# Performance work log

Measured on AMD Instinct MI355X. Metric: run time of the kernel, lower is better.

## Reference

```python
import jax, jax.numpy as jnp
import numpy as np
from jax import lax

EPS = 1e-4  # BatchNorm eps from the module
K = 3       # kernel_size
PAD = 1     # padding


def setup_inputs() -> dict:
    key = jax.random.key(0)
    k1, k2, k3 = jax.random.split(key, 3)
    N, Cin, H, Wd = 32, 256, 56, 56
    Cout = 256
    x = jax.random.normal(k1, (N, Cin, H, Wd), dtype=jnp.float32)
    gamma = jnp.ones((Cin,), dtype=jnp.float32)
    beta_bn = jnp.zeros((Cin,), dtype=jnp.float32)
    W = jax.random.normal(k2, (Cout, Cin, K, K), dtype=jnp.float32) * 0.05
    b = jax.random.normal(k3, (Cout,), dtype=jnp.float32) * 0.01
    return {"x": x, "gamma": gamma, "beta_bn": beta_bn, "W": W, "b": b}


def _conv(x, w, padding):
    return lax.conv_general_dilated(
        x, w, window_strides=(1, 1),
        padding=[(padding, padding), (padding, padding)],
        dimension_numbers=("NCHW", "OIHW", "NCHW"))


def reference(x, gamma, beta_bn, W, b):
    # BatchNorm2d in training mode: batch statistics over (N, H, W), biased var
    mu = jnp.mean(x, axis=(0, 2, 3), keepdims=True)
    var = jnp.var(x, axis=(0, 2, 3), keepdims=True)
    xn = (x - mu) * lax.rsqrt(var + EPS)
    xn = xn * gamma[None, :, None, None] + beta_bn[None, :, None, None]

    # BinActiv: per-pixel channel-mean of |x|, then sign-binarize
    m = jnp.mean(jnp.abs(xn), axis=1, keepdims=True)  # [N,1,H,W]
    xb = jnp.sign(xn)

    # Binarize weights; alpha = L1 norm per output filter / n
    n = W.shape[1] * W.shape[2] * W.shape[3]
    alpha = jnp.sum(jnp.abs(W), axis=(1, 2, 3)) / n  # [Cout]
    Wb = jnp.sign(W)

    y = _conv(xb, Wb, PAD) + b[None, :, None, None]

    # beta map: box filter (stride 1) over channel-mean magnitudes
    box = jnp.full((1, 1, K, K), 1.0 / (K * K), dtype=x.dtype)
    beta_map = _conv(m, box, PAD)  # [N,1,Ho,Wo]

    out = jax.nn.relu(y * beta_map * alpha[None, :, None, None])
    return out
```

## Files before the change

### kernel.cpp

```cpp
#include <hip/hip_runtime.h>
#include <cstdint>
#include <cstddef>

#define N_    32
#define C_    256
#define H_    56
#define W_    56
#define HW_   (H_ * W_)
#define NHW_  (N_ * HW_)
#define COUT_ 256
#define EPS_  1e-4f

__global__ void k_bn_partial(const float* __restrict__ x,
                             float* __restrict__ ps, float* __restrict__ pq) {
    const int c = blockIdx.x >> 3;
    const int s = blockIdx.x & 7;
    const int t = threadIdx.x;
    float sm = 0.f, sq = 0.f;
    for (int n = s * 4; n < s * 4 + 4; ++n) {
        const float4* p = (const float4*)(x + (size_t)(n * C_ + c) * HW_);
        for (int i = t; i < HW_ / 4; i += 256) {
            float4 v = p[i];
            sm += v.x + v.y + v.z + v.w;
            sq += v.x * v.x + v.y * v.y + v.z * v.z + v.w * v.w;
        }
    }
    __shared__ float ls[256], lq[256];
    ls[t] = sm; lq[t] = sq;
    __syncthreads();
    for (int off = 128; off >= 1; off >>= 1) {
        if (t < off) { ls[t] += ls[t + off]; lq[t] += lq[t + off]; }
        __syncthreads();
    }
    if (t == 0) { ps[s * C_ + c] = ls[0]; pq[s * C_ + c] = lq[0]; }
}

__global__ void k_bn_final(const float* __restrict__ ps, const float* __restrict__ pq,
                           const float* __restrict__ gamma, const float* __restrict__ beta,
                           float* __restrict__ a, float* __restrict__ bb) {
    const int c = threadIdx.x;
    float sm = 0.f, sq = 0.f;
    for (int s = 0; s < 8; ++s) { sm += ps[s * C_ + c]; sq += pq[s * C_ + c]; }
    float mu   = sm * (1.f / NHW_);
    float var  = sq * (1.f / NHW_) - mu * mu;
    float rstd = rsqrtf(var + EPS_);
    float g    = gamma[c] * rstd;
    a[c]  = g;
    bb[c] = beta[c] - mu * g;
}

__global__ void k_wpack(const float* __restrict__ Wt, float* __restrict__ alpha,
                        uint64_t* __restrict__ wbits, int* __restrict__ wpopc) {
    const int co = blockIdx.x;
    const int ci = threadIdx.x;
    const int lane = ci & 63, wave = ci >> 6;
    const float* p = Wt + (size_t)(co * C_ + ci) * 9;
    float wv[9];
    float asum = 0.f;
#pragma unroll
    for (int t = 0; t < 9; ++t) { wv[t] = p[t]; asum += fabsf(wv[t]); }
    __shared__ int Pl[9];
    if (ci < 9) Pl[ci] = 0;
    __syncthreads();
#pragma unroll
    for (int t = 0; t < 9; ++t) {
        uint64_t mask = __ballot(wv[t] > 0.f);
        if (lane == 0) {
            wbits[(co * 9 + t) * 4 + wave] = mask;
            atomicAdd(&Pl[t], (int)__popcll(mask));
        }
    }
    __shared__ float red[256];
    red[ci] = asum;
    __syncthreads();
    for (int off = 128; off >= 1; off >>= 1) {
        if (ci < off) red[ci] += red[ci + off];
        __syncthreads();
    }
    if (ci == 0) alpha[co] = red[0] * (1.f / 2304.f);
    if (ci < 9) wpopc[co * 12 + ci] = Pl[ci];
}

__global__ void k_mpack(const float* __restrict__ x, const float* __restrict__ a,
                        const float* __restrict__ bb, uint64_t* __restrict__ xbits,
                        float* __restrict__ m) {
    const int p = blockIdx.x * 256 + threadIdx.x;
    const int n = p / HW_;
    const int hw = p - n * HW_;
    const float* xp = x + (size_t)n * C_ * HW_ + hw;
    float macc = 0.f;
    uint64_t bits[4];
#pragma unroll
    for (int wd = 0; wd < 4; ++wd) {
        uint64_t bw = 0;
#pragma unroll
        for (int j = 0; j < 64; ++j) {
            const int c = wd * 64 + j;
            float xn = fmaf(xp[(size_t)c * HW_], a[c], bb[c]);
            macc += fabsf(xn);
            bw |= (xn > 0.f) ? (1ull << j) : 0ull;
        }
        bits[wd] = bw;
    }
    ulonglong2* xb = (ulonglong2*)(xbits + (size_t)p * 4);
    xb[0] = make_ulonglong2(bits[0], bits[1]);
    xb[1] = make_ulonglong2(bits[2], bits[3]);
    m[p] = macc * (1.f / C_);
}

__global__ void k_box(const float* __restrict__ m, float* __restrict__ beta_map) {
    const int idx = blockIdx.x * 256 + threadIdx.x;
    if (idx >= NHW_) return;
    const int w = idx % W_;
    const int h = (idx / W_) % H_;
    const int n = idx / HW_;
    const float* mp = m + (size_t)n * HW_;
    float s = 0.f;
#pragma unroll
    for (int dh = 0; dh < 3; ++dh) {
        int ih = h + dh - 1;
        if (ih < 0 || ih >= H_) continue;
#pragma unroll
        for (int dw = 0; dw < 3; ++dw) {
            int iw = w + dw - 1;
            if (iw < 0 || iw >= W_) continue;
            s += mp[ih * W_ + iw];
        }
    }
    beta_map[idx] = s * (1.f / 9.f);
}

__global__ void __launch_bounds__(256)
k_conv(const uint64_t* __restrict__ xbits, const uint64_t* __restrict__ wbits,
       const int* __restrict__ wpopc,
       const float* __restrict__ beta_map, const float* __restrict__ alpha,
       const float* __restrict__ bias, float* __restrict__ out) {
    const int nh = blockIdx.x;
    const int n = nh / H_, h = nh % H_;
    const int lane = (int)(threadIdx.x & 63);
    const int wv = __builtin_amdgcn_readfirstlane((int)(threadIdx.x >> 6));
    const int w = lane;
    const bool r0 = (h > 0), r2 = (h < H_ - 1);

    bool cok0 = (w >= 1) && (w < W_);
    bool cok1 = (w < W_);
    bool cok2 = (w < W_ - 1);
    const int nvalid = (1 + (int)r0 + (int)r2) * ((int)cok0 + (int)cok1 + (int)cok2);

    uint64_t xw[9][4];
    const uint64_t* xim = xbits + (size_t)n * HW_ * 4;
#pragma unroll
    for (int dh = 0; dh < 3; ++dh) {
        const bool rok = (dh == 0) ? r0 : (dh == 2) ? r2 : true;
        int ih = h + dh - 1;
        ih = ih < 0 ? 0 : (ih > H_ - 1 ? H_ - 1 : ih);
#pragma unroll
        for (int dw = 0; dw < 3; ++dw) {
            const bool cok = (dw == 0) ? cok0 : (dw == 2) ? cok2 : cok1;
            int iw = w + dw - 1;
            iw = iw < 0 ? 0 : (iw > W_ - 1 ? W_ - 1 : iw);
            const uint64_t* xp = xim + ((size_t)ih * W_ + iw) * 4;
            const bool ok = rok && cok;
#pragma unroll
            for (int wd = 0; wd < 4; ++wd)
                xw[dh * 3 + dw][wd] = ok ? xp[wd] : 0ull;
        }
    }

    const float bm = (w < W_) ? beta_map[(size_t)n * HW_ + (size_t)h * W_ + w] : 0.f;
    float* obase = out + (size_t)n * COUT_ * HW_ + (size_t)h * W_;

    for (int coi = 0; coi < 64; ++coi) {
        const int co = wv * 64 + coi;
        const uint64_t* wq = wbits + (size_t)co * 36;
        const int* pq = wpopc + co * 12;

        int acc0 = 0, acc1 = 0, acc2 = 0, acc3 = 0;
#pragma unroll
        for (int t = 0; t < 9; ++t) {
            acc0 += __popcll(xw[t][0] ^ wq[t * 4 + 0]);
            acc1 += __popcll(xw[t][1] ^ wq[t * 4 + 1]);
            acc2 += __popcll(xw[t][2] ^ wq[t * 4 + 2]);
            acc3 += __popcll(xw[t][3] ^ wq[t * 4 + 3]);
        }
        const int acc = (acc0 + acc1) + (acc2 + acc3);

        int P[9], Ptot = 0;
#pragma unroll
        for (int t = 0; t < 9; ++t) { P[t] = pq[t]; Ptot += P[t]; }
        const int cs0 = (r0 ? P[0] : 0) + P[3] + (r2 ? P[6] : 0);
        const int cs1 = (r0 ? P[1] : 0) + P[4] + (r2 ? P[7] : 0);
        const int cs2 = (r0 ? P[2] : 0) + P[5] + (r2 ? P[8] : 0);
        const int sumv = (cok0 ? cs0 : 0) + (cok1 ? cs1 : 0) + (cok2 ? cs2 : 0);
        const int corr = Ptot - sumv;

        const int dot = 256 * nvalid - 2 * acc + 2 * corr;
        float o = ((float)dot + bias[co]) * bm * alpha[co];
        o = fmaxf(o, 0.f);
        if (w < W_) obase[(size_t)co * HW_ + w] = o;
    }
}

extern "C" void kernel_launch(void* const* d_in, const int* in_sizes, int n_in,
                              void* d_out, int out_size, void* d_ws, size_t ws_size,
                              hipStream_t stream) {
    (void)in_sizes; (void)n_in; (void)out_size; (void)ws_size;
    const float* x     = (const float*)d_in[0];
    const float* gamma = (const float*)d_in[1];
    const float* betab = (const float*)d_in[2];
    const float* Wt    = (const float*)d_in[3];
    const float* b     = (const float*)d_in[4];
    float* out = (float*)d_out;

    uint8_t* base = (uint8_t*)d_ws;
    float*    ps       = (float*)(base + 0);
    float*    pq       = (float*)(base + 8192);
    float*    a        = (float*)(base + 16384);
    float*    bb       = (float*)(base + 17408);
    float*    alpha    = (float*)(base + 18432);
    int*      wpopc    = (int*)(base + 19456);
    uint64_t* wbits    = (uint64_t*)(base + 31744);
    uint64_t* xbits    = (uint64_t*)(base + 105472);
    float*    m        = (float*)(base + 3316736);
    float*    beta_map = (float*)(base + 3718144);

    k_bn_partial<<<2048, 256, 0, stream>>>(x, ps, pq);
    k_bn_final<<<1, 256, 0, stream>>>(ps, pq, gamma, betab, a, bb);
    k_wpack<<<COUT_, 256, 0, stream>>>(Wt, alpha, wbits, wpopc);
    k_mpack<<<NHW_ / 256, 256, 0, stream>>>(x, a, bb, xbits, m);
    k_box<<<(NHW_ + 255) / 256, 256, 0, stream>>>(m, beta_map);
    k_conv<<<N_ * H_, 256, 0, stream>>>(xbits, wbits, wpopc, beta_map, alpha, b, out);
}
```

Measured before the change: 369.4 us.

## Pad bit-packed input, precompute border correction table, flatten conv grid

The packed sign bits of the activations now go into a zero-padded 58x58 image, so the conv kernel loads its 3x3 neighbourhood with no bounds checks or selects. Per-filter border corrections become a 9-entry class table per output channel, built in the weight-pack kernel, which replaces the per-iteration popcount correction arithmetic. The conv grid maps one thread per pixel over flattened NHW with 4 output-channel groups, so lanes no longer idle on the 8 unused columns of each 64-wide row. In exchange there is an extra memset of the padded buffer, and launch bounds of 4 may push the 36-register-pair input window toward spilling.

```diff
diff --git a/kernel.cpp b/kernel.cpp
--- a/kernel.cpp
+++ b/kernel.cpp
@@ -10,6 +10,8 @@
 #define NHW_  (N_ * HW_)
 #define COUT_ 256
 #define EPS_  1e-4f
+#define PW_   58
+#define PIMG_ (PW_ * PW_)
 
 __global__ void k_bn_partial(const float* __restrict__ x,
                              float* __restrict__ ps, float* __restrict__ pq) {
@@ -50,7 +52,7 @@
 }
 
 __global__ void k_wpack(const float* __restrict__ Wt, float* __restrict__ alpha,
-                        uint64_t* __restrict__ wbits, int* __restrict__ wpopc) {
+                        uint64_t* __restrict__ wbits, int* __restrict__ ctab) {
     const int co = blockIdx.x;
     const int ci = threadIdx.x;
     const int lane = ci & 63, wave = ci >> 6;
@@ -78,7 +80,16 @@
         __syncthreads();
     }
     if (ci == 0) alpha[co] = red[0] * (1.f / 2304.f);
-    if (ci < 9) wpopc[co * 12 + ci] = Pl[ci];
+    if (ci < 9) {
+        const int rc = ci / 3, cc = ci % 3;
+        unsigned m9 = (rc == 0 ? 0x007u : 0u) | (rc == 2 ? 0x1C0u : 0u)
+                    | (cc == 0 ? 0x049u : 0u) | (cc == 2 ? 0x124u : 0u);
+        int s = 0;
+#pragma unroll
+        for (int t = 0; t < 9; ++t)
+            if ((m9 >> t) & 1) s += 2 * Pl[t] - 256;
+        ctab[ci * 256 + co] = s;
+    }
 }
 
 __global__ void k_mpack(const float* __restrict__ x, const float* __restrict__ a,
@@ -87,6 +98,8 @@
     const int p = blockIdx.x * 256 + threadIdx.x;
     const int n = p / HW_;
     const int hw = p - n * HW_;
+    const int h = hw / W_;
+    const int w = hw - h * W_;
     const float* xp = x + (size_t)n * C_ * HW_ + hw;
     float macc = 0.f;
     uint64_t bits[4];
@@ -102,7 +115,7 @@
         }
         bits[wd] = bw;
     }
-    ulonglong2* xb = (ulonglong2*)(xbits + (size_t)p * 4);
+    ulonglong2* xb = (ulonglong2*)(xbits + ((size_t)n * PIMG_ + (size_t)(h + 1) * PW_ + (w + 1)) * 4);
     xb[0] = make_ulonglong2(bits[0], bits[1]);
     xb[1] = make_ulonglong2(bits[2], bits[3]);
     m[p] = macc * (1.f / C_);
@@ -130,74 +143,53 @@
     beta_map[idx] = s * (1.f / 9.f);
 }
 
-__global__ void __launch_bounds__(256)
+__global__ void __launch_bounds__(256, 4)
 k_conv(const uint64_t* __restrict__ xbits, const uint64_t* __restrict__ wbits,
-       const int* __restrict__ wpopc,
-       const float* __restrict__ beta_map, const float* __restrict__ alpha,
-       const float* __restrict__ bias, float* __restrict__ out) {
-    const int nh = blockIdx.x;
-    const int n = nh / H_, h = nh % H_;
-    const int lane = (int)(threadIdx.x & 63);
-    const int wv = __builtin_amdgcn_readfirstlane((int)(threadIdx.x >> 6));
-    const int w = lane;
-    const bool r0 = (h > 0), r2 = (h < H_ - 1);
-
-    bool cok0 = (w >= 1) && (w < W_);
-    bool cok1 = (w < W_);
-    bool cok2 = (w < W_ - 1);
-    const int nvalid = (1 + (int)r0 + (int)r2) * ((int)cok0 + (int)cok1 + (int)cok2);
-
-    uint64_t xw[9][4];
-    const uint64_t* xim = xbits + (size_t)n * HW_ * 4;
-#pragma unroll
-    for (int dh = 0; dh < 3; ++dh) {
-        const bool rok = (dh == 0) ? r0 : (dh == 2) ? r2 : true;
-        int ih = h + dh - 1;
-        ih = ih < 0 ? 0 : (ih > H_ - 1 ? H_ - 1 : ih);
+       const int* __restrict__ ctab, const float* __restrict__ beta_map,
+       const float* __restrict__ alpha, const float* __restrict__ bias,
+       float* __restrict__ out) {
+    const int p   = blockIdx.x * 256 + (int)threadIdx.x;
+    const int grp = blockIdx.y;
+    const int n  = p / HW_;
+    const int hw = p - n * HW_;
+    const int h  = hw / W_;
+    const int w  = hw - h * W_;
+
+    const uint64_t* xb = xbits + ((size_t)n * PIMG_ + (size_t)h * PW_ + w) * 4;
+    uint64_t xw[36];
+#pragma unroll
+    for (int dh = 0; dh < 3; ++dh)
 #pragma unroll
         for (int dw = 0; dw < 3; ++dw) {
-            const bool cok = (dw == 0) ? cok0 : (dw == 2) ? cok2 : cok1;
-            int iw = w + dw - 1;
-            iw = iw < 0 ? 0 : (iw > W_ - 1 ? W_ - 1 : iw);
-            const uint64_t* xp = xim + ((size_t)ih * W_ + iw) * 4;
-            const bool ok = rok && cok;
+            const uint64_t* tp = xb + ((size_t)dh * PW_ + dw) * 4;
 #pragma unroll
             for (int wd = 0; wd < 4; ++wd)
-                xw[dh * 3 + dw][wd] = ok ? xp[wd] : 0ull;
-        }
-    }
-
-    const float bm = (w < W_) ? beta_map[(size_t)n * HW_ + (size_t)h * W_ + w] : 0.f;
-    float* obase = out + (size_t)n * COUT_ * HW_ + (size_t)h * W_;
+                xw[(dh * 3 + dw) * 4 + wd] = tp[wd];
+        }
+
+    const int rowcls = (h == 0) ? 0 : ((h == H_ - 1) ? 2 : 1);
+    const int colcls = (w == 0) ? 0 : ((w == W_ - 1) ? 2 : 1);
+    const int* crow = ctab + (rowcls * 3 + colcls) * 256 + grp * 64;
+
+    const float bm = beta_map[p];
+    float* op = out + (size_t)n * COUT_ * HW_ + (size_t)(grp * 64) * HW_ + hw;
 
     for (int coi = 0; coi < 64; ++coi) {
-        const int co = wv * 64 + coi;
+        const int co = grp * 64 + coi;
         const uint64_t* wq = wbits + (size_t)co * 36;
-        const int* pq = wpopc + co * 12;
-
-        int acc0 = 0, acc1 = 0, acc2 = 0, acc3 = 0;
+        int a0 = 0, a1 = 0, a2 = 0, a3 = 0;
 #pragma unroll
         for (int t = 0; t < 9; ++t) {
-            acc0 += __popcll(xw[t][0] ^ wq[t * 4 + 0]);
-            acc1 += __popcll(xw[t][1] ^ wq[t * 4 + 1]);
-            acc2 += __popcll(xw[t][2] ^ wq[t * 4 + 2]);
-            acc3 += __popcll(xw[t][3] ^ wq[t * 4 + 3]);
-        }
-        const int acc = (acc0 + acc1) + (acc2 + acc3);
-
-        int P[9], Ptot = 0;
-#pragma unroll
-        for (int t = 0; t < 9; ++t) { P[t] = pq[t]; Ptot += P[t]; }
-        const int cs0 = (r0 ? P[0] : 0) + P[3] + (r2 ? P[6] : 0);
-        const int cs1 = (r0 ? P[1] : 0) + P[4] + (r2 ? P[7] : 0);
-        const int cs2 = (r0 ? P[2] : 0) + P[5] + (r2 ? P[8] : 0);
-        const int sumv = (cok0 ? cs0 : 0) + (cok1 ? cs1 : 0) + (cok2 ? cs2 : 0);
-        const int corr = Ptot - sumv;
-
-        const int dot = 256 * nvalid - 2 * acc + 2 * corr;
+            a0 += __popcll(xw[t * 4 + 0] ^ wq[t * 4 + 0]);
+            a1 += __popcll(xw[t * 4 + 1] ^ wq[t * 4 + 1]);
+            a2 += __popcll(xw[t * 4 + 2] ^ wq[t * 4 + 2]);
+            a3 += __popcll(xw[t * 4 + 3] ^ wq[t * 4 + 3]);
+        }
+        const int acc = (a0 + a1) + (a2 + a3);
+        const int dot = 2304 - 2 * acc + crow[coi];
         float o = ((float)dot + bias[co]) * bm * alpha[co];
         o = fmaxf(o, 0.f);
-        if (w < W_) obase[(size_t)co * HW_ + w] = o;
+        op[(size_t)coi * HW_] = o;
     }
 }
 
@@ -218,16 +210,17 @@
     float*    a        = (float*)(base + 16384);
     float*    bb       = (float*)(base + 17408);
     float*    alpha    = (float*)(base + 18432);
-    int*      wpopc    = (int*)(base + 19456);
-    uint64_t* wbits    = (uint64_t*)(base + 31744);
-    uint64_t* xbits    = (uint64_t*)(base + 105472);
-    float*    m        = (float*)(base + 3316736);
-    float*    beta_map = (float*)(base + 3718144);
+    int*      ctab     = (int*)(base + 19456);
+    uint64_t* wbits    = (uint64_t*)(base + 28672);
+    uint64_t* xbits    = (uint64_t*)(base + 102400);
+    float*    m        = (float*)(base + 3547136);
+    float*    beta_map = (float*)(base + 3948544);
 
     k_bn_partial<<<2048, 256, 0, stream>>>(x, ps, pq);
     k_bn_final<<<1, 256, 0, stream>>>(ps, pq, gamma, betab, a, bb);
-    k_wpack<<<COUT_, 256, 0, stream>>>(Wt, alpha, wbits, wpopc);
+    k_wpack<<<COUT_, 256, 0, stream>>>(Wt, alpha, wbits, ctab);
+    hipMemsetAsync(xbits, 0, (size_t)N_ * PIMG_ * 4 * sizeof(uint64_t), stream);
     k_mpack<<<NHW_ / 256, 256, 0, stream>>>(x, a, bb, xbits, m);
     k_box<<<(NHW_ + 255) / 256, 256, 0, stream>>>(m, beta_map);
-    k_conv<<<N_ * H_, 256, 0, stream>>>(xbits, wbits, wpopc, beta_map, alpha, b, out);
-}
+    k_conv<<<dim3(NHW_ / 256, 4), 256, 0, stream>>>(xbits, wbits, ctab, beta_map, alpha, b, out);
+}
```

Measured after the change: 337.0 us. 1.1x faster.
